# Kernel tuning notes

Measured on AMD Instinct MI355X. Metric: run time of the kernel, lower is better.

The kernel has to match this reference:

```python
import jax, jax.numpy as jnp
import numpy as np

B, T, D = 4, 1024, 2048      # batch, tokens, d_model (= Linear out_features)
N, S, H = 8, 8, 8            # n_concepts, gate_rank, degen_rank
ETA = 1.0


def setup_inputs() -> dict:
    key = jax.random.key(0)
    ks = jax.random.split(key, 9)
    return {
        "x": jax.random.normal(ks[0], (B, T, D), jnp.float32),
        # selector params (kaiming-ish then / d_model^2 -> small); use /D for nontrivial values
        "select_weight": jax.random.normal(ks[1], (N, D, S), jnp.float32) / D,
        "select_mean_diff": jax.random.normal(ks[2], (N, D), jnp.float32) / D,
        "imp_center": jax.random.normal(ks[3], (N,), jnp.float32),
        "imp_slope": jax.random.normal(ks[4], (N,), jnp.float32) * 5.0,
        "lora_update": jax.random.normal(ks[5], (N, D, H), jnp.float32) * 0.02,
        "lora_degen": jax.random.normal(ks[6], (N, D, H), jnp.float32) * 0.02,
        "bias_w": jax.random.normal(ks[7], (N, D), jnp.float32) * 0.02,
        "debias_w": jax.random.normal(ks[8], (N, D), jnp.float32) * 0.02,
    }


def reference(x, select_weight, select_mean_diff, imp_center, imp_slope,
              lora_update, lora_degen, bias_w, debias_w):
    # ---- SimpleSelectorOutProp ----
    # x: [B,T,D]; x_diff: [B,N,T,D]  (x.unsqueeze(1) - mean_diff[None,:,None,:])
    x_diff = x[:, None, :, :] - select_mean_diff[None, :, None, :]
    x_diff = x_diff / jnp.linalg.norm(x_diff, axis=3, keepdims=True)
    # cont: [B,N,T,S] = einsum('nds,bntd->bnts')**2
    cont = jnp.einsum('nds,bntd->bnts', select_weight, x_diff) ** 2
    score = cont.sum(axis=-1)                                   # [B,N,T]
    gate = jax.nn.sigmoid(imp_slope[None, :, None] * (score - imp_center[None, :, None]))
    sel_scale = gate.max(axis=1)[..., None]                     # [B,T,1] (max over concepts)
    sel_idx = gate.argmax(axis=1)                               # [B,T] int (top-1 concept)

    # ---- top-1 concept gather + low-rank update ----
    debias = jnp.take(debias_w, sel_idx, axis=0)                # [B,T,D]
    bias = jnp.take(bias_w, sel_idx, axis=0)                    # [B,T,D]
    upd = jnp.take(lora_update, sel_idx, axis=0)                # [B,T,D,H]
    dgn = jnp.take(lora_degen, sel_idx, axis=0)                 # [B,T,D,H]

    x_debias = x - debias
    mod_x = jnp.einsum('btdh,btd->bth', upd, x_debias)          # [B,T,H]
    degen_up = jnp.einsum('btdh,bth->btd', dgn, mod_x)          # [B,T,D]
    mod_x_bias = ETA * (bias + degen_up)

    # gated residual blend: (1 - s) * x + s * mod_x_bias
    return (1.0 - sel_scale) * x + sel_scale * mod_x_bias
```

## Files before the change

### kernel.cpp

```cpp
#include <hip/hip_runtime.h>
#include <math.h>

typedef unsigned short u16;
typedef unsigned int   u32;
typedef unsigned long long u64;
typedef __attribute__((ext_vector_type(4))) unsigned short u16x4;
typedef __attribute__((ext_vector_type(8))) unsigned short bf16x8;
typedef __attribute__((ext_vector_type(8))) short sh8;
typedef __attribute__((ext_vector_type(4))) float f32x4;

#define BT     4096
#define D      2048
#define NC     8
#define NCOL   144
#define KSPLIT 8
#define KR     (D / KSPLIT)

__device__ __forceinline__ float bf2f(u16 v) {
    u32 u = ((u32)v) << 16;
    float f; __builtin_memcpy(&f, &u, 4); return f;
}
__device__ __forceinline__ u16 f2bf(float f) {
    u32 u; __builtin_memcpy(&u, &f, 4);
    u += 0x7fffu + ((u >> 16) & 1);
    return (u16)(u >> 16);
}

__device__ __forceinline__ int detect_fp32(const void* xv) {
    const u16* p = (const u16*)xv;
    int l = threadIdx.x & 63;
    bool bad = false;
#pragma unroll
    for (int i = 0; i < 4; i++) {
        float v = bf2f(p[l * 4 + i]);
        if (!(fabsf(v) < 1e4f)) bad = true;
    }
    return __ballot(bad) != 0ull;
}

template<int DT> struct IO;
template<> struct IO<0> {
    static __device__ __forceinline__ float ld1(const void* p, size_t i) {
        return bf2f(((const u16*)p)[i]);
    }
    static __device__ __forceinline__ void ld4(const void* p, size_t i, float* o) {
        u16x4 v = *(const u16x4*)((const u16*)p + i);
#pragma unroll
        for (int k = 0; k < 4; k++) o[k] = bf2f(v[k]);
    }
    static __device__ __forceinline__ void ld8(const void* p, size_t i, float* o) {
        bf16x8 v = *(const bf16x8*)((const u16*)p + i);
#pragma unroll
        for (int k = 0; k < 8; k++) o[k] = bf2f(v[k]);
    }
    static __device__ __forceinline__ void st4(void* p, size_t i, const float* v) {
        u16x4 o;
#pragma unroll
        for (int k = 0; k < 4; k++) o[k] = f2bf(v[k]);
        *(u16x4*)((u16*)p + i) = o;
    }
    static __device__ __forceinline__ u16 ldbf(const void* p, size_t i) {
        return ((const u16*)p)[i];
    }
    static __device__ __forceinline__ sh8 afrag(const void* p, size_t i) {
        return *(const sh8*)((const u16*)p + i);
    }
};
template<> struct IO<1> {
    static __device__ __forceinline__ float ld1(const void* p, size_t i) {
        return ((const float*)p)[i];
    }
    static __device__ __forceinline__ void ld4(const void* p, size_t i, float* o) {
        f32x4 a = *(const f32x4*)((const float*)p + i);
#pragma unroll
        for (int k = 0; k < 4; k++) o[k] = a[k];
    }
    static __device__ __forceinline__ void ld8(const void* p, size_t i, float* o) {
        f32x4 a = *(const f32x4*)((const float*)p + i);
        f32x4 b = *(const f32x4*)((const float*)p + i + 4);
#pragma unroll
        for (int k = 0; k < 4; k++) { o[k] = a[k]; o[4 + k] = b[k]; }
    }
    static __device__ __forceinline__ void st4(void* p, size_t i, const float* v) {
        f32x4 a;
#pragma unroll
        for (int k = 0; k < 4; k++) a[k] = v[k];
        *(f32x4*)((float*)p + i) = a;
    }
    static __device__ __forceinline__ u16 ldbf(const void* p, size_t i) {
        return f2bf(((const float*)p)[i]);
    }
    static __device__ __forceinline__ sh8 afrag(const void* p, size_t i) {
        f32x4 a = *(const f32x4*)((const float*)p + i);
        f32x4 b = *(const f32x4*)((const float*)p + i + 4);
        sh8 r;
#pragma unroll
        for (int k = 0; k < 4; k++) {
            r[k]     = (short)f2bf(a[k]);
            r[4 + k] = (short)f2bf(b[k]);
        }
        return r;
    }
};

template<int DT>
__device__ __forceinline__ void prep_part(const void* selW, const void* upd,
                                          const void* mu, u16* __restrict__ WtT) {
    int idx = blockIdx.x * 256 + threadIdx.x;
    int j = idx >> 8, d0 = (idx & 255) * 8;
    bf16x8 v;
    if (j < 64) {
        int n = j >> 3, s = j & 7;
#pragma unroll
        for (int i = 0; i < 8; i++) v[i] = IO<DT>::ldbf(selW, ((size_t)n * D + d0 + i) * 8 + s);
    } else if (j < 128) {
        int n = (j - 64) >> 3, h = j & 7;
#pragma unroll
        for (int i = 0; i < 8; i++) v[i] = IO<DT>::ldbf(upd, ((size_t)n * D + d0 + i) * 8 + h);
    } else if (j < 136) {
#pragma unroll
        for (int i = 0; i < 8; i++) v[i] = IO<DT>::ldbf(mu, (size_t)(j - 128) * D + d0 + i);
    } else {
#pragma unroll
        for (int i = 0; i < 8; i++) v[i] = 0;
    }
    *(bf16x8*)(WtT + (size_t)j * D + d0) = v;
}

template<int DT>
__device__ __forceinline__ void consts_part(const void* W, const void* mu,
                                            const void* upd, const void* deb,
                                            float* gOff, float* gMu2, float* gUb) {
    int bid = blockIdx.x - 144;
    int n = bid >> 3, t = threadIdx.x;
    int d = (bid & 7) * 256 + t;

    float mud = IO<DT>::ld1(mu,  (size_t)n * D + d);
    float dbd = IO<DT>::ld1(deb, (size_t)n * D + d);
    float m2 = mud * mud;
    float wv[8], uv[8], o[8], u[8];
    IO<DT>::ld8(W,   ((size_t)n * D + d) * 8, wv);
    IO<DT>::ld8(upd, ((size_t)n * D + d) * 8, uv);
#pragma unroll
    for (int s = 0; s < 8; s++) { o[s] = wv[s] * mud; u[s] = uv[s] * dbd; }

#pragma unroll
    for (int i = 1; i < 64; i <<= 1) {
        m2 += __shfl_xor(m2, i, 64);
#pragma unroll
        for (int s = 0; s < 8; s++) {
            o[s] += __shfl_xor(o[s], i, 64);
            u[s] += __shfl_xor(u[s], i, 64);
        }
    }
    __shared__ float red[4][17];
    int wave = t >> 6, lane = t & 63;
    if (lane == 0) {
        red[wave][0] = m2;
#pragma unroll
        for (int s = 0; s < 8; s++) { red[wave][1 + s] = o[s]; red[wave][9 + s] = u[s]; }
    }
    __syncthreads();
    if (t < 17) {
        float acc = red[0][t] + red[1][t] + red[2][t] + red[3][t];
        if (t == 0)      atomicAdd(&gMu2[n], acc);
        else if (t < 9)  atomicAdd(&gOff[n * 8 + t - 1], acc);
        else             atomicAdd(&gUb[n * 8 + t - 9], acc);
    }
}

template<int DT>
__device__ __forceinline__ void dgnb_part(const void* dgn, u16* __restrict__ dgnb) {
    int idx = (blockIdx.x - 208) * 256 + threadIdx.x;
    float v[8];
    IO<DT>::ld8(dgn, (size_t)idx * 8, v);
    bf16x8 o;
#pragma unroll
    for (int k = 0; k < 8; k++) o[k] = f2bf(v[k]);
    *(bf16x8*)(dgnb + (size_t)idx * 8) = o;
}

__global__ __launch_bounds__(256) void k_prep(
    const void* x, const void* selW, const void* upd, const void* mu,
    const void* deb, const void* dgn, u16* WtT,
    float* gOff, float* gMu2, float* gUb, u16* dgnb) {
    int f = detect_fp32(x);
    if (blockIdx.x < 144) {
        if (f) prep_part<1>(selW, upd, mu, WtT); else prep_part<0>(selW, upd, mu, WtT);
    } else if (blockIdx.x < 208) {
        if (f) consts_part<1>(selW, mu, upd, deb, gOff, gMu2, gUb);
        else   consts_part<0>(selW, mu, upd, deb, gOff, gMu2, gUb);
    } else {
        if (f) dgnb_part<1>(dgn, dgnb); else dgnb_part<0>(dgn, dgnb);
    }
}

template<int DT>
__device__ __forceinline__ void gemm_body(const void* X, const u16* __restrict__ WtT,
                                          float* __restrict__ Pslices,
                                          float* __restrict__ sumx2p) {
    const int t = threadIdx.x;
    const int w = t >> 6, l = t & 63;
    const int m = l & 15, q = l >> 4;
    const int tok0 = blockIdx.x * 64 + w * 16;
    const int p = blockIdx.y;
    const int k0 = p * KR;

    const size_t aoff = (size_t)(tok0 + m) * D + k0 + q * 8;
    const u16* bp = WtT + (size_t)m * D + k0 + q * 8;

    f32x4 acc[9];
#pragma unroll
    for (int ct = 0; ct < 9; ct++) acc[ct] = (f32x4){0.f, 0.f, 0.f, 0.f};
    float s2 = 0.f;

#pragma unroll 2
    for (int ks = 0; ks < KR / 32; ks++) {
        sh8 a = IO<DT>::afrag(X, aoff + ks * 32);
        sh8 b[9];
#pragma unroll
        for (int ct = 0; ct < 9; ct++)
            b[ct] = *(const sh8*)(bp + (size_t)ct * 16 * D + ks * 32);
#pragma unroll
        for (int i = 0; i < 8; i++) {
            float xv = bf2f((u16)a[i]);
            s2 = fmaf(xv, xv, s2);
        }
#pragma unroll
        for (int ct = 0; ct < 9; ct++)
            acc[ct] = __builtin_amdgcn_mfma_f32_16x16x32_bf16(a, b[ct], acc[ct], 0, 0, 0);
    }

    s2 += __shfl_xor(s2, 16, 64);
    s2 += __shfl_xor(s2, 32, 64);
    if (l < 16) sumx2p[(size_t)p * BT + tok0 + l] = s2;

    float* Ps = Pslices + (size_t)p * BT * NCOL;
#pragma unroll
    for (int ct = 0; ct < 9; ct++)
#pragma unroll
        for (int r = 0; r < 4; r++)
            Ps[(size_t)(tok0 + q * 4 + r) * NCOL + ct * 16 + m] = acc[ct][r];
}
__global__ __launch_bounds__(256) void k_gemm(const void* X, const u16* WtT,
                                              float* Pslices, float* sumx2p) {
    if (detect_fp32(X)) gemm_body<1>(X, WtT, Pslices, sumx2p);
    else                gemm_body<0>(X, WtT, Pslices, sumx2p);
}

template<int DT>
__device__ __forceinline__ void gate_body(
    const float* __restrict__ Pslices, const float* __restrict__ sumx2p,
    const void* CENTER, const void* SLOPE,
    const float* __restrict__ OFF, const float* __restrict__ MU2,
    const float* __restrict__ UB,
    float* __restrict__ svals, int* __restrict__ cs, float* __restrict__ mxs) {
    const int g = blockIdx.x * 256 + threadIdx.x;
    const int tok = g >> 3, n = g & 7;

    f32x4 pa = {0.f, 0.f, 0.f, 0.f}, pb = {0.f, 0.f, 0.f, 0.f};
    float mdot = 0.f, s2 = 0.f;
#pragma unroll
    for (int p = 0; p < KSPLIT; p++) {
        const float* pr = Pslices + ((size_t)p * BT + tok) * NCOL;
        f32x4 a = *(const f32x4*)(pr + 8 * n);
        f32x4 b = *(const f32x4*)(pr + 8 * n + 4);
#pragma unroll
        for (int k = 0; k < 4; k++) { pa[k] += a[k]; pb[k] += b[k]; }
        mdot += pr[128 + n];
        s2 += sumx2p[(size_t)p * BT + tok];
    }

    float norm2 = s2 - 2.f * mdot + MU2[n];
    float sc = 0.f;
#pragma unroll
    for (int s = 0; s < 4; s++) {
        float d0 = pa[s] - OFF[8 * n + s];
        float d1 = pb[s] - OFF[8 * n + 4 + s];
        sc += d0 * d0 + d1 * d1;
    }
    sc /= norm2;
    float zv = IO<DT>::ld1(SLOPE, n) * (sc - IO<DT>::ld1(CENTER, n));
    int iv = n;
#pragma unroll
    for (int i = 1; i < 8; i <<= 1) {
        float z2 = __shfl_xor(zv, i, 64);
        int   i2 = __shfl_xor(iv, i, 64);
        if (z2 > zv || (z2 == zv && i2 < iv)) { zv = z2; iv = i2; }
    }
    const int c = iv;
    float mxv = 0.f;
#pragma unroll
    for (int p = 0; p < KSPLIT; p++)
        mxv += Pslices[((size_t)p * BT + tok) * NCOL + 64 + 8 * c + n];
    mxs[(size_t)tok * 8 + n] = mxv - UB[c * 8 + n];
    if (n == 0) { svals[tok] = 1.f / (1.f + expf(-zv)); cs[tok] = c; }
}
__global__ __launch_bounds__(256) void k_gate(
    const float* Pslices, const float* sumx2p, const void* X,
    const void* CENTER, const void* SLOPE,
    const float* OFF, const float* MU2, const float* UB,
    float* svals, int* cs, float* mxs) {
    if (detect_fp32(X)) gate_body<1>(Pslices, sumx2p, CENTER, SLOPE, OFF, MU2, UB, svals, cs, mxs);
    else                gate_body<0>(Pslices, sumx2p, CENTER, SLOPE, OFF, MU2, UB, svals, cs, mxs);
}

template<int DT>
__device__ __forceinline__ void blend_body(
    const void* X, const float* __restrict__ svals, const int* __restrict__ cs,
    const float* __restrict__ mxs, const u16* __restrict__ DGNB,
    const void* BIAS, void* OUT) {
    const int tok = blockIdx.x >> 1;
    const int d0 = (blockIdx.x & 1) * 1024 + threadIdx.x * 4;

    const int c = cs[tok];
    const float sval = svals[tok];
    f32x4 mxa = *(const f32x4*)(mxs + (size_t)tok * 8);
    f32x4 mxb = *(const f32x4*)(mxs + (size_t)tok * 8 + 4);

    float xf[4], bv[4], ov[4];
    IO<DT>::ld4(X,    (size_t)tok * D + d0, xf);
    IO<DT>::ld4(BIAS, (size_t)c * D + d0, bv);
#pragma unroll
    for (int i = 0; i < 4; i++) {
        bf16x8 v = *(const bf16x8*)(DGNB + ((size_t)c * D + d0 + i) * 8);
        float du = bf2f(v[0]) * mxa[0] + bf2f(v[1]) * mxa[1]
                 + bf2f(v[2]) * mxa[2] + bf2f(v[3]) * mxa[3]
                 + bf2f(v[4]) * mxb[0] + bf2f(v[5]) * mxb[1]
                 + bf2f(v[6]) * mxb[2] + bf2f(v[7]) * mxb[3];
        ov[i] = (1.f - sval) * xf[i] + sval * (bv[i] + du);
    }
    IO<DT>::st4(OUT, (size_t)tok * D + d0, ov);
}
__global__ __launch_bounds__(256) void k_blend(
    const void* X, const float* svals, const int* cs, const float* mxs,
    const u16* DGNB, const void* BIAS, void* OUT) {
    if (detect_fp32(X)) blend_body<1>(X, svals, cs, mxs, DGNB, BIAS, OUT);
    else                blend_body<0>(X, svals, cs, mxs, DGNB, BIAS, OUT);
}

extern "C" void kernel_launch(void* const* d_in, const int* in_sizes, int n_in,
                              void* d_out, int out_size, void* d_ws, size_t ws_size,
                              hipStream_t stream) {
    const void* x      = d_in[0];
    const void* selW   = d_in[1];
    const void* mu     = d_in[2];
    const void* center = d_in[3];
    const void* slope  = d_in[4];
    const void* upd    = d_in[5];
    const void* dgn    = d_in[6];
    const void* biasW  = d_in[7];
    const void* debW   = d_in[8];

    float* Pslices = (float*)d_out;
    char* ws = (char*)d_ws;
    float* sumx2p = (float*)ws;
    float* svals  = (float*)(ws + 131072);
    int*   cs     = (int*)  (ws + 147456);
    float* mxs    = (float*)(ws + 163840);
    u16*   WtT    = (u16*)  (ws + 294912);
    u16*   dgnb   = (u16*)  (ws + 884736);
    float* consts = (float*)(ws + 1146880);
    float* off = consts, *mu2 = consts + 64, *ub = consts + 72;

    hipMemsetAsync(consts, 0, 576, stream);
    k_prep <<<272, 256, 0, stream>>>(x, selW, upd, mu, debW, dgn,
                                     WtT, off, mu2, ub, dgnb);
    k_gemm <<<dim3(BT / 64, KSPLIT), 256, 0, stream>>>(x, WtT, Pslices, sumx2p);
    k_gate <<<BT * NC / 256, 256, 0, stream>>>(Pslices, sumx2p, x, center, slope,
                                               off, mu2, ub, svals, cs, mxs);
    k_blend<<<BT * 2, 256, 0, stream>>>(x, svals, cs, mxs, dgnb, biasW, d_out);
}
```

Measured before the change: 143.0 us.

## Fuse GEMM, gate and blend into one kernel with in-block K-split reduction

The separate gemm, gate and blend kernels become a single kernel. Each 512-thread block handles 16 tokens, and its 8 waves split the K dimension. Partial projections are reduced in shared memory instead of being written to and reread from a global Pslices buffer, and the top-1 gate and the gated blend run in the same block. The atomic accumulation of per-concept constants and its memset are replaced by per-block partial writes that the fused kernel sums itself. This removes a large global round trip and two launches. The costs are that each block loops serially over 16 tokens in the blend, and that only 256 blocks are launched, which limits latency hiding.

```diff
diff --git a/kernel.cpp b/kernel.cpp
--- a/kernel.cpp
+++ b/kernel.cpp
@@ -13,8 +13,10 @@
 #define D      2048
 #define NC     8
 #define NCOL   144
-#define KSPLIT 8
-#define KR     (D / KSPLIT)
+#define NW     8
+#define KR     (D / NW)
+#define TPB    16
+#define LPAD   (NCOL + 4)
 
 __device__ __forceinline__ float bf2f(u16 v) {
     u32 u = ((u32)v) << 16;
@@ -130,10 +132,10 @@
 template<int DT>
 __device__ __forceinline__ void consts_part(const void* W, const void* mu,
                                             const void* upd, const void* deb,
-                                            float* gOff, float* gMu2, float* gUb) {
-    int bid = blockIdx.x - 144;
-    int n = bid >> 3, t = threadIdx.x;
-    int d = (bid & 7) * 256 + t;
+                                            float* __restrict__ gPart) {
+    int pid = blockIdx.x - 144;
+    int n = pid >> 3, t = threadIdx.x;
+    int d = (pid & 7) * 256 + t;
 
     float mud = IO<DT>::ld1(mu,  (size_t)n * D + d);
     float dbd = IO<DT>::ld1(deb, (size_t)n * D + d);
@@ -163,9 +165,7 @@
     __syncthreads();
     if (t < 17) {
         float acc = red[0][t] + red[1][t] + red[2][t] + red[3][t];
-        if (t == 0)      atomicAdd(&gMu2[n], acc);
-        else if (t < 9)  atomicAdd(&gOff[n * 8 + t - 1], acc);
-        else             atomicAdd(&gUb[n * 8 + t - 9], acc);
+        gPart[pid * 17 + t] = acc;
     }
 }
 
@@ -182,29 +182,42 @@
 
 __global__ __launch_bounds__(256) void k_prep(
     const void* x, const void* selW, const void* upd, const void* mu,
-    const void* deb, const void* dgn, u16* WtT,
-    float* gOff, float* gMu2, float* gUb, u16* dgnb) {
+    const void* deb, const void* dgn, u16* WtT, float* gPart, u16* dgnb) {
     int f = detect_fp32(x);
     if (blockIdx.x < 144) {
         if (f) prep_part<1>(selW, upd, mu, WtT); else prep_part<0>(selW, upd, mu, WtT);
     } else if (blockIdx.x < 208) {
-        if (f) consts_part<1>(selW, mu, upd, deb, gOff, gMu2, gUb);
-        else   consts_part<0>(selW, mu, upd, deb, gOff, gMu2, gUb);
+        if (f) consts_part<1>(selW, mu, upd, deb, gPart);
+        else   consts_part<0>(selW, mu, upd, deb, gPart);
     } else {
         if (f) dgnb_part<1>(dgn, dgnb); else dgnb_part<0>(dgn, dgnb);
     }
 }
 
 template<int DT>
-__device__ __forceinline__ void gemm_body(const void* X, const u16* __restrict__ WtT,
-                                          float* __restrict__ Pslices,
-                                          float* __restrict__ sumx2p) {
+__device__ __forceinline__ void fused_body(
+    const void* X, const u16* __restrict__ WtT, const float* __restrict__ gPart,
+    const u16* __restrict__ DGNB, const void* BIAS,
+    const void* CENTER, const void* SLOPE, void* OUT,
+    float (*LP)[TPB][LPAD], float (*LS2)[TPB],
+    float (*cOFF)[8], float (*cUB)[8], float* cMU2,
+    float (*mxL)[8], float* svalL, int* cL) {
+
     const int t = threadIdx.x;
     const int w = t >> 6, l = t & 63;
     const int m = l & 15, q = l >> 4;
-    const int tok0 = blockIdx.x * 64 + w * 16;
-    const int p = blockIdx.y;
-    const int k0 = p * KR;
+    const int tok0 = blockIdx.x * TPB;
+    const int k0 = w * KR;
+
+    if (t < 136) {
+        int n = t / 17, k = t % 17;
+        float s = 0.f;
+#pragma unroll
+        for (int j = 0; j < 8; j++) s += gPart[(n * 8 + j) * 17 + k];
+        if (k == 0)      cMU2[n] = s;
+        else if (k < 9)  cOFF[n][k - 1] = s;
+        else             cUB[n][k - 9] = s;
+    }
 
     const size_t aoff = (size_t)(tok0 + m) * D + k0 + q * 8;
     const u16* bp = WtT + (size_t)m * D + k0 + q * 8;
@@ -233,110 +246,97 @@
 
     s2 += __shfl_xor(s2, 16, 64);
     s2 += __shfl_xor(s2, 32, 64);
-    if (l < 16) sumx2p[(size_t)p * BT + tok0 + l] = s2;
-
-    float* Ps = Pslices + (size_t)p * BT * NCOL;
+    if (l < 16) LS2[w][l] = s2;
+
 #pragma unroll
     for (int ct = 0; ct < 9; ct++)
 #pragma unroll
         for (int r = 0; r < 4; r++)
-            Ps[(size_t)(tok0 + q * 4 + r) * NCOL + ct * 16 + m] = acc[ct][r];
-}
-__global__ __launch_bounds__(256) void k_gemm(const void* X, const u16* WtT,
-                                              float* Pslices, float* sumx2p) {
-    if (detect_fp32(X)) gemm_body<1>(X, WtT, Pslices, sumx2p);
-    else                gemm_body<0>(X, WtT, Pslices, sumx2p);
-}
-
-template<int DT>
-__device__ __forceinline__ void gate_body(
-    const float* __restrict__ Pslices, const float* __restrict__ sumx2p,
-    const void* CENTER, const void* SLOPE,
-    const float* __restrict__ OFF, const float* __restrict__ MU2,
-    const float* __restrict__ UB,
-    float* __restrict__ svals, int* __restrict__ cs, float* __restrict__ mxs) {
-    const int g = blockIdx.x * 256 + threadIdx.x;
-    const int tok = g >> 3, n = g & 7;
-
-    f32x4 pa = {0.f, 0.f, 0.f, 0.f}, pb = {0.f, 0.f, 0.f, 0.f};
-    float mdot = 0.f, s2 = 0.f;
-#pragma unroll
-    for (int p = 0; p < KSPLIT; p++) {
-        const float* pr = Pslices + ((size_t)p * BT + tok) * NCOL;
-        f32x4 a = *(const f32x4*)(pr + 8 * n);
-        f32x4 b = *(const f32x4*)(pr + 8 * n + 4);
-#pragma unroll
-        for (int k = 0; k < 4; k++) { pa[k] += a[k]; pb[k] += b[k]; }
-        mdot += pr[128 + n];
-        s2 += sumx2p[(size_t)p * BT + tok];
-    }
-
-    float norm2 = s2 - 2.f * mdot + MU2[n];
-    float sc = 0.f;
-#pragma unroll
-    for (int s = 0; s < 4; s++) {
-        float d0 = pa[s] - OFF[8 * n + s];
-        float d1 = pb[s] - OFF[8 * n + 4 + s];
-        sc += d0 * d0 + d1 * d1;
-    }
-    sc /= norm2;
-    float zv = IO<DT>::ld1(SLOPE, n) * (sc - IO<DT>::ld1(CENTER, n));
-    int iv = n;
-#pragma unroll
-    for (int i = 1; i < 8; i <<= 1) {
-        float z2 = __shfl_xor(zv, i, 64);
-        int   i2 = __shfl_xor(iv, i, 64);
-        if (z2 > zv || (z2 == zv && i2 < iv)) { zv = z2; iv = i2; }
-    }
-    const int c = iv;
-    float mxv = 0.f;
-#pragma unroll
-    for (int p = 0; p < KSPLIT; p++)
-        mxv += Pslices[((size_t)p * BT + tok) * NCOL + 64 + 8 * c + n];
-    mxs[(size_t)tok * 8 + n] = mxv - UB[c * 8 + n];
-    if (n == 0) { svals[tok] = 1.f / (1.f + expf(-zv)); cs[tok] = c; }
-}
-__global__ __launch_bounds__(256) void k_gate(
-    const float* Pslices, const float* sumx2p, const void* X,
-    const void* CENTER, const void* SLOPE,
-    const float* OFF, const float* MU2, const float* UB,
-    float* svals, int* cs, float* mxs) {
-    if (detect_fp32(X)) gate_body<1>(Pslices, sumx2p, CENTER, SLOPE, OFF, MU2, UB, svals, cs, mxs);
-    else                gate_body<0>(Pslices, sumx2p, CENTER, SLOPE, OFF, MU2, UB, svals, cs, mxs);
-}
-
-template<int DT>
-__device__ __forceinline__ void blend_body(
-    const void* X, const float* __restrict__ svals, const int* __restrict__ cs,
-    const float* __restrict__ mxs, const u16* __restrict__ DGNB,
-    const void* BIAS, void* OUT) {
-    const int tok = blockIdx.x >> 1;
-    const int d0 = (blockIdx.x & 1) * 1024 + threadIdx.x * 4;
-
-    const int c = cs[tok];
-    const float sval = svals[tok];
-    f32x4 mxa = *(const f32x4*)(mxs + (size_t)tok * 8);
-    f32x4 mxb = *(const f32x4*)(mxs + (size_t)tok * 8 + 4);
-
-    float xf[4], bv[4], ov[4];
-    IO<DT>::ld4(X,    (size_t)tok * D + d0, xf);
-    IO<DT>::ld4(BIAS, (size_t)c * D + d0, bv);
-#pragma unroll
-    for (int i = 0; i < 4; i++) {
-        bf16x8 v = *(const bf16x8*)(DGNB + ((size_t)c * D + d0 + i) * 8);
-        float du = bf2f(v[0]) * mxa[0] + bf2f(v[1]) * mxa[1]
-                 + bf2f(v[2]) * mxa[2] + bf2f(v[3]) * mxa[3]
-                 + bf2f(v[4]) * mxb[0] + bf2f(v[5]) * mxb[1]
-                 + bf2f(v[6]) * mxb[2] + bf2f(v[7]) * mxb[3];
-        ov[i] = (1.f - sval) * xf[i] + sval * (bv[i] + du);
-    }
-    IO<DT>::st4(OUT, (size_t)tok * D + d0, ov);
-}
-__global__ __launch_bounds__(256) void k_blend(
-    const void* X, const float* svals, const int* cs, const float* mxs,
-    const u16* DGNB, const void* BIAS, void* OUT) {
-    if (detect_fp32(X)) blend_body<1>(X, svals, cs, mxs, DGNB, BIAS, OUT);
-    else                blend_body<0>(X, svals, cs, mxs, DGNB, BIAS, OUT);
+            LP[w][q * 4 + r][ct * 16 + m] = acc[ct][r];
+    __syncthreads();
+
+    if (t < 128) {
+        const int tok = t >> 3, n = t & 7;
+        float sx2 = 0.f;
+#pragma unroll
+        for (int u = 0; u < NW; u++) sx2 += LS2[u][tok];
+
+        float pa[8];
+#pragma unroll
+        for (int s = 0; s < 8; s++) {
+            float v = 0.f;
+#pragma unroll
+            for (int u = 0; u < NW; u++) v += LP[u][tok][n * 8 + s];
+            pa[s] = v;
+        }
+        float mdot = 0.f;
+#pragma unroll
+        for (int u = 0; u < NW; u++) mdot += LP[u][tok][128 + n];
+
+        float norm2 = sx2 - 2.f * mdot + cMU2[n];
+        float sc = 0.f;
+#pragma unroll
+        for (int s = 0; s < 8; s++) {
+            float dd = pa[s] - cOFF[n][s];
+            sc += dd * dd;
+        }
+        sc /= norm2;
+        float zv = IO<DT>::ld1(SLOPE, n) * (sc - IO<DT>::ld1(CENTER, n));
+        int iv = n;
+#pragma unroll
+        for (int i = 1; i < 8; i <<= 1) {
+            float z2 = __shfl_xor(zv, i, 64);
+            int   i2 = __shfl_xor(iv, i, 64);
+            if (z2 > zv || (z2 == zv && i2 < iv)) { zv = z2; iv = i2; }
+        }
+        const int c = iv;
+        float mxv = 0.f;
+#pragma unroll
+        for (int u = 0; u < NW; u++) mxv += LP[u][tok][64 + c * 8 + n];
+        mxL[tok][n] = mxv - cUB[c][n];
+        if (n == 0) { svalL[tok] = 1.f / (1.f + expf(-zv)); cL[tok] = c; }
+    }
+    __syncthreads();
+
+    const int d0 = t * 4;
+    for (int tok = 0; tok < TPB; ++tok) {
+        const int c = cL[tok];
+        const float sval = svalL[tok];
+        float mxa[8];
+#pragma unroll
+        for (int h = 0; h < 8; h++) mxa[h] = mxL[tok][h];
+
+        const size_t trow = (size_t)(tok0 + tok) * D;
+        float xf[4], bv[4], ov[4];
+        IO<DT>::ld4(X,    trow + d0, xf);
+        IO<DT>::ld4(BIAS, (size_t)c * D + d0, bv);
+#pragma unroll
+        for (int i = 0; i < 4; i++) {
+            bf16x8 v = *(const bf16x8*)(DGNB + ((size_t)c * D + d0 + i) * 8);
+            float du = bf2f(v[0]) * mxa[0] + bf2f(v[1]) * mxa[1]
+                     + bf2f(v[2]) * mxa[2] + bf2f(v[3]) * mxa[3]
+                     + bf2f(v[4]) * mxa[4] + bf2f(v[5]) * mxa[5]
+                     + bf2f(v[6]) * mxa[6] + bf2f(v[7]) * mxa[7];
+            ov[i] = (1.f - sval) * xf[i] + sval * (bv[i] + du);
+        }
+        IO<DT>::st4(OUT, trow + d0, ov);
+    }
+}
+
+__global__ __launch_bounds__(512) void k_fused(
+    const void* X, const u16* WtT, const float* gPart, const u16* DGNB,
+    const void* BIAS, const void* CENTER, const void* SLOPE, void* OUT) {
+    __shared__ float LP[NW][TPB][LPAD];
+    __shared__ float LS2[NW][TPB];
+    __shared__ float cOFF[8][8], cUB[8][8], cMU2[8];
+    __shared__ float mxL[TPB][8], svalL[TPB];
+    __shared__ int   cL[TPB];
+    if (detect_fp32(X))
+        fused_body<1>(X, WtT, gPart, DGNB, BIAS, CENTER, SLOPE, OUT,
+                      LP, LS2, cOFF, cUB, cMU2, mxL, svalL, cL);
+    else
+        fused_body<0>(X, WtT, gPart, DGNB, BIAS, CENTER, SLOPE, OUT,
+                      LP, LS2, cOFF, cUB, cMU2, mxL, svalL, cL);
 }
 
 extern "C" void kernel_launch(void* const* d_in, const int* in_sizes, int n_in,
@@ -352,22 +352,11 @@
     const void* biasW  = d_in[7];
     const void* debW   = d_in[8];
 
-    float* Pslices = (float*)d_out;
     char* ws = (char*)d_ws;
-    float* sumx2p = (float*)ws;
-    float* svals  = (float*)(ws + 131072);
-    int*   cs     = (int*)  (ws + 147456);
-    float* mxs    = (float*)(ws + 163840);
-    u16*   WtT    = (u16*)  (ws + 294912);
-    u16*   dgnb   = (u16*)  (ws + 884736);
-    float* consts = (float*)(ws + 1146880);
-    float* off = consts, *mu2 = consts + 64, *ub = consts + 72;
-
-    hipMemsetAsync(consts, 0, 576, stream);
-    k_prep <<<272, 256, 0, stream>>>(x, selW, upd, mu, debW, dgn,
-                                     WtT, off, mu2, ub, dgnb);
-    k_gemm <<<dim3(BT / 64, KSPLIT), 256, 0, stream>>>(x, WtT, Pslices, sumx2p);
-    k_gate <<<BT * NC / 256, 256, 0, stream>>>(Pslices, sumx2p, x, center, slope,
-                                               off, mu2, ub, svals, cs, mxs);
-    k_blend<<<BT * 2, 256, 0, stream>>>(x, svals, cs, mxs, dgnb, biasW, d_out);
-}
+    u16*   WtT   = (u16*)ws;
+    u16*   dgnb  = (u16*)(ws + 589824);
+    float* gPart = (float*)(ws + 851968);
+
+    k_prep <<<272, 256, 0, stream>>>(x, selW, upd, mu, debW, dgn, WtT, gPart, dgnb);
+    k_fused<<<BT / TPB, 512, 0, stream>>>(x, WtT, gPart, dgnb, biasW, center, slope, d_out);
+}
```

Result: faster. 124.9 us (-12.7%).
